# Kernel tuning notes

Measured on AMD Instinct MI355X. Metric: run time of the kernel, lower is better.

## Reference

```python
import jax, jax.numpy as jnp
import numpy as np

N = 262144
C_IN = 128
C_OUT = 128
K = 9


def setup_inputs() -> dict:
    key = jax.random.key(0)
    k1, k2, k3, k4 = jax.random.split(key, 4)
    features = jax.random.normal(k1, (N, C_IN), dtype=jnp.float32)
    neigh_idx = jax.random.randint(k2, (N, K), 0, N, dtype=jnp.int64)
    # nn.Linear(9*in_channels, out_channels): weight [out, 9*in], bias [out]
    fan_in = K * C_IN
    W = jax.random.normal(k3, (C_OUT, fan_in), dtype=jnp.float32) / np.sqrt(fan_in)
    b = jax.random.normal(k4, (C_OUT,), dtype=jnp.float32) * 0.01
    return {"features": features, "neigh_idx": neigh_idx, "W": W, "b": b}


def reference(features, neigh_idx, W, b):
    n = features.shape[0]
    # pad row of zeros at index n; redirect -1 neighbors to it
    feat_padded = jnp.concatenate([features, jnp.zeros((1, features.shape[1]), features.dtype)], axis=0)
    gather_idx = jnp.where(neigh_idx == -1, n, neigh_idx)
    col = feat_padded[gather_idx]              # [N, 9, C_in]
    col_flat = col.reshape(n, -1)              # [N, 9*C_in]
    return col_flat @ W.T + b                  # [N, C_out]
```

## Files before the change

kernel.cpp:

```cpp
#include <hip/hip_runtime.h>


#define NPTS    262144
#define CIN     128
#define COUT    128
#define KNBR    9
#define KDIM    (KNBR * CIN)
#define NKS     (KDIM / 16)
#define NFRAGS  (NKS * 4)
#define MT      256

typedef __bf16  bf16x8 __attribute__((ext_vector_type(8)));
typedef float   f32x4  __attribute__((ext_vector_type(4)));
typedef float   f32x16 __attribute__((ext_vector_type(16)));

__global__ __launch_bounds__(256) void convert_feat_kernel(const float* __restrict__ f,
                                                           __bf16* __restrict__ fb) {
    size_t i = ((size_t)blockIdx.x * 256 + threadIdx.x) * 8;
    f32x4 a = *(const f32x4*)(f + i);
    f32x4 b = *(const f32x4*)(f + i + 4);
    bf16x8 o;
#pragma unroll
    for (int k = 0; k < 4; ++k) { o[k] = (__bf16)a[k]; o[k + 4] = (__bf16)b[k]; }
    *(bf16x8*)(fb + i) = o;
}

__global__ __launch_bounds__(256) void pack_w_kernel(const float* __restrict__ W,
                                                     __bf16* __restrict__ Wp,
                                                     float* __restrict__ zrow_f,
                                                     __bf16* __restrict__ zrow_b) {
    if (blockIdx.x == NFRAGS / 4) {
        int t = threadIdx.x;
        if (t < 128) zrow_f[t] = 0.f;
        else         zrow_b[t - 128] = (__bf16)0.f;
        return;
    }
    int t    = blockIdx.x * 256 + threadIdx.x;
    int lane = t & 63;
    int frag = t >> 6;
    int nt = frag & 3;
    int ks = frag >> 2;
    int n  = nt * 32 + (lane & 31);
    int k0 = ks * 16 + (lane >> 5) * 8;
    const f32x4* src = (const f32x4*)(W + (size_t)n * KDIM + k0);
    f32x4 v0 = src[0], v1 = src[1];
    bf16x8 o;
#pragma unroll
    for (int i = 0; i < 4; ++i) { o[i] = (__bf16)v0[i]; o[i + 4] = (__bf16)v1[i]; }
    *(bf16x8*)(Wp + (size_t)frag * 512 + lane * 8) = o;
}

template <bool BF16A, typename AT>
__global__ __launch_bounds__(256, 2) void qconv_kernel(
    const AT*     __restrict__ featA,
    const int*    __restrict__ nidx,
    const __bf16* __restrict__ Wp,
    const AT*     __restrict__ zrow,
    const float*  __restrict__ bias,
    float*        __restrict__ out)
{
    const int tid  = threadIdx.x;
    const int lane = tid & 63;
    const int wave = tid >> 6;
    const int l31  = lane & 31;
    const int half = lane >> 5;
    const int rb   = blockIdx.x * MT;
    const int p0   = rb + wave * 32 + l31;
    const int p1   = p0 + 128;

    const int* n0 = nidx + (size_t)p0 * KNBR;
    const int* n1 = nidx + (size_t)p1 * KNBR;
    const AT* pa0[KNBR];
    const AT* pa1[KNBR];
#pragma unroll
    for (int j = 0; j < KNBR; ++j) {
        int g0 = n0[j], g1 = n1[j];
        pa0[j] = (g0 >= 0) ? featA + (size_t)g0 * CIN : zrow;
        pa1[j] = (g1 >= 0) ? featA + (size_t)g1 * CIN : zrow;
    }

    f32x16 acc[8];
#pragma unroll
    for (int a = 0; a < 8; ++a)
#pragma unroll
        for (int i = 0; i < 16; ++i) acc[a][i] = 0.f;

    constexpr int AD = BF16A ? 4 : 2;
    bf16x8 AbB[BF16A ? AD : 1][2];
    f32x4  AbF[BF16A ? 1 : AD][2][2];
    bf16x8 Bb[3][4];

    auto issueA = [&](int t) {
        const int j = t >> 3, kk = t & 7;
        const int off = kk * 16 + half * 8;
        if constexpr (BF16A) {
            AbB[t % AD][0] = *(const bf16x8*)((const __bf16*)pa0[j] + off);
            AbB[t % AD][1] = *(const bf16x8*)((const __bf16*)pa1[j] + off);
        } else {
            AbF[t % AD][0][0] = *(const f32x4*)((const float*)pa0[j] + off);
            AbF[t % AD][0][1] = *(const f32x4*)((const float*)pa0[j] + off + 4);
            AbF[t % AD][1][0] = *(const f32x4*)((const float*)pa1[j] + off);
            AbF[t % AD][1][1] = *(const f32x4*)((const float*)pa1[j] + off + 4);
        }
    };
    auto getA = [&](int t, int tile) -> bf16x8 {
        if constexpr (BF16A) {
            return AbB[t % AD][tile];
        } else {
            f32x4 x = AbF[t % AD][tile][0], y = AbF[t % AD][tile][1];
            bf16x8 o;
#pragma unroll
            for (int k = 0; k < 4; ++k) { o[k] = (__bf16)x[k]; o[k + 4] = (__bf16)y[k]; }
            return o;
        }
    };
    auto issueB = [&](int t) {
#pragma unroll
        for (int nt = 0; nt < 4; ++nt)
            Bb[t % 3][nt] = *(const bf16x8*)(Wp + (size_t)(t * 4 + nt) * 512 + lane * 8);
    };

    issueA(0); issueA(1);
    if constexpr (BF16A) { issueA(2); issueA(3); }
    issueB(0); issueB(1);

#pragma unroll
    for (int t = 0; t < NKS; ++t) {
        if (t + 2 < NKS) issueB(t + 2);
        bf16x8 a0 = getA(t, 0);
        bf16x8 a1 = getA(t, 1);
#pragma unroll
        for (int nt = 0; nt < 4; ++nt) {
            acc[nt]     = __builtin_amdgcn_mfma_f32_32x32x16_bf16(a0, Bb[t % 3][nt], acc[nt], 0, 0, 0);
            acc[4 + nt] = __builtin_amdgcn_mfma_f32_32x32x16_bf16(a1, Bb[t % 3][nt], acc[4 + nt], 0, 0, 0);
        }
        if (t + AD < NKS) issueA(t + AD);
    }

#pragma unroll
    for (int nt = 0; nt < 4; ++nt) {
        const int col = nt * 32 + l31;
        const float bv = bias[col];
#pragma unroll
        for (int r = 0; r < 16; ++r) {
            const int row = (r & 3) + 8 * (r >> 2) + 4 * half;
            out[(size_t)(rb + wave * 32 + row) * COUT + col]       = acc[nt][r] + bv;
            out[(size_t)(rb + 128 + wave * 32 + row) * COUT + col] = acc[4 + nt][r] + bv;
        }
    }
}

extern "C" void kernel_launch(void* const* d_in, const int* in_sizes, int n_in,
                              void* d_out, int out_size, void* d_ws, size_t ws_size,
                              hipStream_t stream) {
    const float* feat = (const float*)d_in[0];
    const int*   nidx = (const int*)d_in[1];
    const float* W    = (const float*)d_in[2];
    const float* bias = (const float*)d_in[3];
    float*       out  = (float*)d_out;

    const size_t FEATB_BYTES = (size_t)NPTS * CIN * 2;
    const size_t WP_BYTES    = (size_t)NFRAGS * 512 * 2;

    if (ws_size >= FEATB_BYTES + WP_BYTES + 1024) {
        __bf16* featb  = (__bf16*)d_ws;
        __bf16* Wp     = (__bf16*)((char*)d_ws + FEATB_BYTES);
        float*  zrow_f = (float*)((char*)d_ws + FEATB_BYTES + WP_BYTES);
        __bf16* zrow_b = (__bf16*)((char*)d_ws + FEATB_BYTES + WP_BYTES + 512);
        convert_feat_kernel<<<NPTS * CIN / (256 * 8), 256, 0, stream>>>(feat, featb);
        pack_w_kernel<<<NFRAGS / 4 + 1, 256, 0, stream>>>(W, Wp, zrow_f, zrow_b);
        qconv_kernel<true, __bf16><<<NPTS / MT, 256, 0, stream>>>(featb, nidx, Wp, zrow_b, bias, out);
    } else {
        __bf16* Wp     = (__bf16*)d_ws;
        float*  zrow_f = (float*)((char*)d_ws + WP_BYTES);
        __bf16* zrow_b = (__bf16*)((char*)d_ws + WP_BYTES + 512);
        pack_w_kernel<<<NFRAGS / 4 + 1, 256, 0, stream>>>(W, Wp, zrow_f, zrow_b);
        qconv_kernel<false, float><<<NPTS / MT, 256, 0, stream>>>(feat, nidx, Wp, zrow_f, bias, out);
    }
}
```

Before: 372.3 us.

## Stage gathered neighbor rows into LDS via async global_load_lds double buffering

Replaces per-lane register gathers of neighbor feature rows with direct global-to-LDS async loads (global_load_lds) into a swizzled, double-buffered per-wave LDS region. Explicit vmcnt waits and sched_barriers pipeline the staging of the next half-chunk against MFMA work on the current one, and neighbor indices are loaded one column ahead. The fp32 fallback path is replaced with a naive kernel and Wp is padded so the B prefetch can run past the end. This costs 64KB of LDS per block, which may limit occupancy, and relies on hand-tuned waitcnt values being correct.

After: 367.4 us. No clear change (-1.3%).

```diff
diff --git a/kernel.cpp b/kernel.cpp
--- a/kernel.cpp
+++ b/kernel.cpp
@@ -5,14 +5,17 @@
 #define CIN     128
 #define COUT    128
 #define KNBR    9
-#define KDIM    (KNBR * CIN)
-#define NKS     (KDIM / 16)
-#define NFRAGS  (NKS * 4)
+#define KDIM    1152
+#define NKS     72
+#define NFRAGS  288
+#define NFRAGS_PAD 296
 #define MT      256
 
 typedef __bf16  bf16x8 __attribute__((ext_vector_type(8)));
 typedef float   f32x4  __attribute__((ext_vector_type(4)));
 typedef float   f32x16 __attribute__((ext_vector_type(16)));
+
+#define VMCNT(n) (((n) & 0xF) | (((n) >> 4) << 14) | (0xF << 8) | (7 << 4))
 
 __global__ __launch_bounds__(256) void convert_feat_kernel(const float* __restrict__ f,
                                                            __bf16* __restrict__ fb) {
@@ -27,12 +30,10 @@
 
 __global__ __launch_bounds__(256) void pack_w_kernel(const float* __restrict__ W,
                                                      __bf16* __restrict__ Wp,
-                                                     float* __restrict__ zrow_f,
                                                      __bf16* __restrict__ zrow_b) {
     if (blockIdx.x == NFRAGS / 4) {
         int t = threadIdx.x;
-        if (t < 128) zrow_f[t] = 0.f;
-        else         zrow_b[t - 128] = (__bf16)0.f;
+        if (t < CIN) zrow_b[t] = (__bf16)0.f;
         return;
     }
     int t    = blockIdx.x * 256 + threadIdx.x;
@@ -50,33 +51,32 @@
     *(bf16x8*)(Wp + (size_t)frag * 512 + lane * 8) = o;
 }
 
-template <bool BF16A, typename AT>
 __global__ __launch_bounds__(256, 2) void qconv_kernel(
-    const AT*     __restrict__ featA,
+    const __bf16* __restrict__ featb,
     const int*    __restrict__ nidx,
     const __bf16* __restrict__ Wp,
-    const AT*     __restrict__ zrow,
+    const __bf16* __restrict__ zrow,
     const float*  __restrict__ bias,
     float*        __restrict__ out)
 {
+    __shared__ __align__(16) char lds_raw[4 * 2 * 2 * 4096];
+
     const int tid  = threadIdx.x;
     const int lane = tid & 63;
     const int wave = tid >> 6;
     const int l31  = lane & 31;
     const int half = lane >> 5;
     const int rb   = blockIdx.x * MT;
-    const int p0   = rb + wave * 32 + l31;
-    const int p1   = p0 + 128;
-
-    const int* n0 = nidx + (size_t)p0 * KNBR;
-    const int* n1 = nidx + (size_t)p1 * KNBR;
-    const AT* pa0[KNBR];
-    const AT* pa1[KNBR];
-#pragma unroll
-    for (int j = 0; j < KNBR; ++j) {
-        int g0 = n0[j], g1 = n1[j];
-        pa0[j] = (g0 >= 0) ? featA + (size_t)g0 * CIN : zrow;
-        pa1[j] = (g1 >= 0) ? featA + (size_t)g1 * CIN : zrow;
+    char* myLds = lds_raw + wave * 16384;
+
+    const int srow = lane >> 3;
+    const int schk = lane & 7;
+
+    const int* ia[8];
+#pragma unroll
+    for (int n = 0; n < 8; ++n) {
+        int rg = rb + (n >> 2) * 128 + wave * 32 + (n & 3) * 8 + srow;
+        ia[n] = nidx + (size_t)rg * KNBR;
     }
 
     f32x16 acc[8];
@@ -85,33 +85,27 @@
 #pragma unroll
         for (int i = 0; i < 16; ++i) acc[a][i] = 0.f;
 
-    constexpr int AD = BF16A ? 4 : 2;
-    bf16x8 AbB[BF16A ? AD : 1][2];
-    f32x4  AbF[BF16A ? 1 : AD][2][2];
+    const __bf16* Pst[8];
+    int NPidx[8];
     bf16x8 Bb[3][4];
 
-    auto issueA = [&](int t) {
-        const int j = t >> 3, kk = t & 7;
-        const int off = kk * 16 + half * 8;
-        if constexpr (BF16A) {
-            AbB[t % AD][0] = *(const bf16x8*)((const __bf16*)pa0[j] + off);
-            AbB[t % AD][1] = *(const bf16x8*)((const __bf16*)pa1[j] + off);
-        } else {
-            AbF[t % AD][0][0] = *(const f32x4*)((const float*)pa0[j] + off);
-            AbF[t % AD][0][1] = *(const f32x4*)((const float*)pa0[j] + off + 4);
-            AbF[t % AD][1][0] = *(const f32x4*)((const float*)pa1[j] + off);
-            AbF[t % AD][1][1] = *(const f32x4*)((const float*)pa1[j] + off + 4);
-        }
-    };
-    auto getA = [&](int t, int tile) -> bf16x8 {
-        if constexpr (BF16A) {
-            return AbB[t % AD][tile];
-        } else {
-            f32x4 x = AbF[t % AD][tile][0], y = AbF[t % AD][tile][1];
-            bf16x8 o;
-#pragma unroll
-            for (int k = 0; k < 4; ++k) { o[k] = (__bf16)x[k]; o[k + 4] = (__bf16)y[k]; }
-            return o;
+    auto convertP = [&](void) {
+#pragma unroll
+        for (int n = 0; n < 8; ++n)
+            Pst[n] = (NPidx[n] >= 0) ? featb + (size_t)NPidx[n] * CIN : zrow;
+    };
+    auto stage_chunk = [&](int c) {
+        const int buf  = c & 1;
+        const int eoff = (c & 1) * 64 + (schk ^ srow) * 8;
+#pragma unroll
+        for (int n = 0; n < 8; ++n) {
+            const int T = n >> 2, i = n & 3;
+            const __bf16* g = Pst[n] + eoff;
+            char* dst = myLds + buf * 8192 + T * 4096 + i * 1024;
+            __builtin_amdgcn_global_load_lds(
+                (const __attribute__((address_space(1))) void*)g,
+                (__attribute__((address_space(3))) void*)dst,
+                16, 0, 0);
         }
     };
     auto issueB = [&](int t) {
@@ -119,22 +113,62 @@
         for (int nt = 0; nt < 4; ++nt)
             Bb[t % 3][nt] = *(const bf16x8*)(Wp + (size_t)(t * 4 + nt) * 512 + lane * 8);
     };
-
-    issueA(0); issueA(1);
-    if constexpr (BF16A) { issueA(2); issueA(3); }
+    auto readA = [&](int buf, int T, int ksl) -> bf16x8 {
+        const int s = (ksl * 2 + half) ^ (l31 & 7);
+        return *(const bf16x8*)(myLds + buf * 8192 + T * 4096 + l31 * 128 + s * 16);
+    };
+
+#pragma unroll
+    for (int n = 0; n < 8; ++n) NPidx[n] = ia[n][0];
+    convertP();
+    __builtin_amdgcn_sched_barrier(0);
+    stage_chunk(0);
+    __builtin_amdgcn_sched_barrier(0);
     issueB(0); issueB(1);
 
 #pragma unroll
-    for (int t = 0; t < NKS; ++t) {
-        if (t + 2 < NKS) issueB(t + 2);
-        bf16x8 a0 = getA(t, 0);
-        bf16x8 a1 = getA(t, 1);
-#pragma unroll
-        for (int nt = 0; nt < 4; ++nt) {
-            acc[nt]     = __builtin_amdgcn_mfma_f32_32x32x16_bf16(a0, Bb[t % 3][nt], acc[nt], 0, 0, 0);
-            acc[4 + nt] = __builtin_amdgcn_mfma_f32_32x32x16_bf16(a1, Bb[t % 3][nt], acc[4 + nt], 0, 0, 0);
-        }
-        if (t + AD < NKS) issueA(t + AD);
+    for (int j = 0; j < KNBR; ++j) {
+        __builtin_amdgcn_sched_barrier(0);
+        if (j == 0) __builtin_amdgcn_s_waitcnt(VMCNT(8));
+        else        __builtin_amdgcn_s_waitcnt(VMCNT(16));
+        __builtin_amdgcn_sched_barrier(0);
+        stage_chunk(2 * j + 1);
+        __builtin_amdgcn_sched_barrier(0);
+        {
+            const int jn = (j + 1 < KNBR) ? j + 1 : KNBR - 1;
+#pragma unroll
+            for (int n = 0; n < 8; ++n) NPidx[n] = ia[n][jn];
+#pragma unroll
+            for (int ksl = 0; ksl < 4; ++ksl) {
+                const int t = j * 8 + ksl;
+                issueB(t + 2);
+                bf16x8 a0 = readA(0, 0, ksl);
+                bf16x8 a1 = readA(0, 1, ksl);
+#pragma unroll
+                for (int nt = 0; nt < 4; ++nt) {
+                    acc[nt]     = __builtin_amdgcn_mfma_f32_32x32x16_bf16(a0, Bb[t % 3][nt], acc[nt], 0, 0, 0);
+                    acc[4 + nt] = __builtin_amdgcn_mfma_f32_32x32x16_bf16(a1, Bb[t % 3][nt], acc[4 + nt], 0, 0, 0);
+                }
+            }
+        }
+        __builtin_amdgcn_sched_barrier(0);
+        __builtin_amdgcn_s_waitcnt(VMCNT(24));
+        __builtin_amdgcn_sched_barrier(0);
+        convertP();
+        stage_chunk(2 * j + 2);
+        __builtin_amdgcn_sched_barrier(0);
+#pragma unroll
+        for (int ksl = 4; ksl < 8; ++ksl) {
+            const int t = j * 8 + ksl;
+            issueB(t + 2);
+            bf16x8 a0 = readA(1, 0, ksl - 4);
+            bf16x8 a1 = readA(1, 1, ksl - 4);
+#pragma unroll
+            for (int nt = 0; nt < 4; ++nt) {
+                acc[nt]     = __builtin_amdgcn_mfma_f32_32x32x16_bf16(a0, Bb[t % 3][nt], acc[nt], 0, 0, 0);
+                acc[4 + nt] = __builtin_amdgcn_mfma_f32_32x32x16_bf16(a1, Bb[t % 3][nt], acc[4 + nt], 0, 0, 0);
+            }
+        }
     }
 
 #pragma unroll
@@ -148,6 +182,21 @@
             out[(size_t)(rb + 128 + wave * 32 + row) * COUT + col] = acc[4 + nt][r] + bv;
         }
     }
+}
+
+__global__ void qconv_naive(const float* __restrict__ feat, const int* __restrict__ nidx,
+                            const float* __restrict__ W, const float* __restrict__ bias,
+                            float* __restrict__ out) {
+    int p = blockIdx.x, c = threadIdx.x;
+    float s = bias[c];
+    for (int j = 0; j < KNBR; ++j) {
+        int g = nidx[(size_t)p * KNBR + j];
+        if (g < 0) continue;
+        const float* fr = feat + (size_t)g * CIN;
+        const float* wr = W + (size_t)c * KDIM + j * CIN;
+        for (int k = 0; k < CIN; ++k) s += fr[k] * wr[k];
+    }
+    out[(size_t)p * COUT + c] = s;
 }
 
 extern "C" void kernel_launch(void* const* d_in, const int* in_sizes, int n_in,
@@ -160,21 +209,16 @@
     float*       out  = (float*)d_out;
 
     const size_t FEATB_BYTES = (size_t)NPTS * CIN * 2;
-    const size_t WP_BYTES    = (size_t)NFRAGS * 512 * 2;
-
-    if (ws_size >= FEATB_BYTES + WP_BYTES + 1024) {
+    const size_t WP_BYTES    = (size_t)NFRAGS_PAD * 512 * 2;
+
+    if (ws_size >= FEATB_BYTES + WP_BYTES + 512) {
         __bf16* featb  = (__bf16*)d_ws;
         __bf16* Wp     = (__bf16*)((char*)d_ws + FEATB_BYTES);
-        float*  zrow_f = (float*)((char*)d_ws + FEATB_BYTES + WP_BYTES);
-        __bf16* zrow_b = (__bf16*)((char*)d_ws + FEATB_BYTES + WP_BYTES + 512);
+        __bf16* zrow_b = (__bf16*)((char*)d_ws + FEATB_BYTES + WP_BYTES);
         convert_feat_kernel<<<NPTS * CIN / (256 * 8), 256, 0, stream>>>(feat, featb);
-        pack_w_kernel<<<NFRAGS / 4 + 1, 256, 0, stream>>>(W, Wp, zrow_f, zrow_b);
-        qconv_kernel<true, __bf16><<<NPTS / MT, 256, 0, stream>>>(featb, nidx, Wp, zrow_b, bias, out);
+        pack_w_kernel<<<NFRAGS / 4 + 1, 256, 0, stream>>>(W, Wp, zrow_b);
+        qconv_kernel<<<NPTS / MT, 256, 0, stream>>>(featb, nidx, Wp, zrow_b, bias, out);
     } else {
-        __bf16* Wp     = (__bf16*)d_ws;
-        float*  zrow_f = (float*)((char*)d_ws + WP_BYTES);
-        __bf16* zrow_b = (__bf16*)((char*)d_ws + WP_BYTES + 512);
-        pack_w_kernel<<<NFRAGS / 4 + 1, 256, 0, stream>>>(W, Wp, zrow_f, zrow_b);
-        qconv_kernel<false, float><<<NPTS / MT, 256, 0, stream>>>(feat, nidx, Wp, zrow_f, bias, out);
-    }
-}
+        qconv_naive<<<NPTS, COUT, 0, stream>>>(feat, nidx, W, bias, out);
+    }
+}
```
